# Kernel tuning notes

Measured on AMD Instinct MI355X. Metric: run time of the kernel, lower is better.

Reference implementation:

```python
import jax, jax.numpy as jnp
import numpy as np

BASE_RES = 0.2
RES_FACTOR = (1.0 - BASE_RES) * 0.9
N_ATOMS = 1024
LATENT = 128
WINDOW = 512
HOP = WINDOW // 2
RES_SAMPLES = 32768
N_FRAMES = RES_SAMPLES // HOP  # 128


def setup_inputs() -> dict:
    key = jax.random.key(0)
    ks = jax.random.split(key, 6)
    x = jax.random.normal(ks[0], (16, 64, LATENT), dtype=jnp.float32)
    W_sel = jax.random.normal(ks[1], (N_ATOMS, LATENT), dtype=jnp.float32) * 0.1
    b_sel = jnp.zeros((N_ATOMS,), dtype=jnp.float32)
    W_mom = jax.random.normal(ks[2], (N_FRAMES, LATENT), dtype=jnp.float32) * 0.1
    b_mom = jnp.zeros((N_FRAMES,), dtype=jnp.float32)
    atoms = jax.random.normal(ks[3], (N_ATOMS, RES_SAMPLES), dtype=jnp.float32) * 0.01
    return {"x": x, "W_sel": W_sel, "b_sel": b_sel, "W_mom": W_mom, "b_mom": b_mom, "atoms": atoms}


def _hann_periodic(n):
    # torch.hann_window default (periodic=True)
    return 0.5 * (1.0 - jnp.cos(2.0 * jnp.pi * jnp.arange(n) / n))


def reference(x, W_sel, b_sel, W_mom, b_mom, atoms):
    # momentum: sigmoid -> affine -> log-cumsum-exp decay per frame
    mom = BASE_RES + jax.nn.sigmoid(jnp.einsum('bel,fl->bef', x, W_mom) + b_mom) * RES_FACTOR
    mom = jnp.exp(jnp.cumsum(jnp.log(1e-12 + mom), axis=-1))  # (B,E,F)

    # softmax atom selection and mixing
    sel = jax.nn.softmax(jnp.einsum('bel,al->bea', x, W_sel) + b_sel, axis=-1)
    res = jnp.einsum('bea,as->bes', sel, atoms)  # (B,E,S)

    # windowed_audio: pad by hop, unfold, apply hann window
    padded = jnp.pad(res, ((0, 0), (0, 0), (0, HOP)))
    idx = jnp.arange(N_FRAMES)[:, None] * HOP + jnp.arange(WINDOW)[None, :]
    frames = padded[..., idx] * _hann_periodic(WINDOW)  # (B,E,F,W)

    # per-frame unit norm, then momentum scaling
    norm = jnp.linalg.norm(frames, axis=-1, keepdims=True)
    frames = frames / (norm + 1e-8)
    frames = frames * mom[..., None]

    # overlap-add with hop = WINDOW//2 (no extra window)
    B, E = frames.shape[0], frames.shape[1]
    first = frames[..., :HOP].reshape(B, E, -1)
    second = frames[..., HOP:].reshape(B, E, -1)
    out = jnp.pad(first, ((0, 0), (0, 0), (0, HOP))) + jnp.pad(second, ((0, 0), (0, 0), (HOP, 0)))
    return out[..., :RES_SAMPLES], mom
```

## Files before the change

### kernel.cpp

```cpp
#include <hip/hip_runtime.h>


typedef __attribute__((ext_vector_type(8))) short short8;
typedef __attribute__((ext_vector_type(4))) float f32x4;

typedef __attribute__((address_space(1))) void GV;
typedef __attribute__((address_space(3))) void LV;

__device__ __forceinline__ unsigned short f2bf(float f) {
    union { float f; unsigned u; } c; c.f = f;
    unsigned u = c.u;
    u = (u + 0x7FFFu + ((u >> 16) & 1u)) >> 16;
    return (unsigned short)u;
}
__device__ __forceinline__ float bf2f(unsigned short h) {
    union { unsigned u; float f; } c; c.u = ((unsigned)h) << 16; return c.f;
}

__global__ __launch_bounds__(256) void k_convert(
        const float* __restrict__ x, const float* __restrict__ Wsel,
        const float* __restrict__ Wmom,
        unsigned short* __restrict__ xbf, unsigned short* __restrict__ wbf,
        float* __restrict__ WmomT) {
    const int i = (blockIdx.x * 256 + threadIdx.x) * 4;
    {
        float4 v = *(const float4*)(x + i);
        uint2 q;
        q.x = (unsigned)f2bf(v.x) | ((unsigned)f2bf(v.y) << 16);
        q.y = (unsigned)f2bf(v.z) | ((unsigned)f2bf(v.w) << 16);
        *(uint2*)(xbf + i) = q;
    }
    {
        float4 v = *(const float4*)(Wsel + i);
        uint2 q;
        q.x = (unsigned)f2bf(v.x) | ((unsigned)f2bf(v.y) << 16);
        q.y = (unsigned)f2bf(v.z) | ((unsigned)f2bf(v.w) << 16);
        *(uint2*)(wbf + i) = q;
    }
    if (blockIdx.x < 8) {
        const int f  = blockIdx.x * 16 + (threadIdx.x >> 4);
        const int kc = (threadIdx.x & 15) * 8;
        float4 a = *(const float4*)(Wmom + (size_t)f * 128 + kc);
        float4 b = *(const float4*)(Wmom + (size_t)f * 128 + kc + 4);
        WmomT[(kc + 0) * 128 + f] = a.x; WmomT[(kc + 1) * 128 + f] = a.y;
        WmomT[(kc + 2) * 128 + f] = a.z; WmomT[(kc + 3) * 128 + f] = a.w;
        WmomT[(kc + 4) * 128 + f] = b.x; WmomT[(kc + 5) * 128 + f] = b.y;
        WmomT[(kc + 6) * 128 + f] = b.z; WmomT[(kc + 7) * 128 + f] = b.w;
    }
}

__global__ __launch_bounds__(256) void k_head_gemm(
        const unsigned short* __restrict__ A, const unsigned short* __restrict__ Bm,
        float* __restrict__ logits) {
    __shared__ __align__(16) unsigned short lA[128 * 32];
    __shared__ __align__(16) unsigned short lB[128 * 32];
    const int tid = threadIdx.x;
    const int wave = tid >> 6;
    const int lane = tid & 63;
    const int l15 = lane & 15, quad = lane >> 4;
    const int i0 = blockIdx.x * 128;
    const int j0 = blockIdx.y * 128;
    const int wi = wave >> 1, wj = wave & 1;
    const int rsel = lane >> 2;
    const int koff = (lane & 3) * 8;

    f32x4 acc[4][4] = {};

    for (int kt = 0; kt < 4; ++kt) {
        const int kbase = kt * 32;
#pragma unroll
        for (int c = 0; c < 2; ++c) {
            const int row = c * 64 + wave * 16 + rsel;
            const unsigned short* ga = A + (size_t)(i0 + row) * 128 + kbase + koff;
            const unsigned short* gb = Bm + (size_t)(j0 + row) * 128 + kbase + koff;
            unsigned short* la = lA + (c * 64 + wave * 16) * 32;
            unsigned short* lb = lB + (c * 64 + wave * 16) * 32;
            __builtin_amdgcn_global_load_lds((GV*)ga, (LV*)la, 16, 0, 0);
            __builtin_amdgcn_global_load_lds((GV*)gb, (LV*)lb, 16, 0, 0);
        }
        __syncthreads();

        short8 af[4], bf[4];
#pragma unroll
        for (int ti = 0; ti < 4; ++ti)
            af[ti] = *(const short8*)(lA + (wi * 64 + ti * 16 + l15) * 32 + quad * 8);
#pragma unroll
        for (int tj = 0; tj < 4; ++tj)
            bf[tj] = *(const short8*)(lB + (wj * 64 + tj * 16 + l15) * 32 + quad * 8);
#pragma unroll
        for (int ti = 0; ti < 4; ++ti)
#pragma unroll
            for (int tj = 0; tj < 4; ++tj)
                acc[ti][tj] = __builtin_amdgcn_mfma_f32_16x16x32_bf16(
                    af[ti], bf[tj], acc[ti][tj], 0, 0, 0);
        __syncthreads();
    }

#pragma unroll
    for (int ti = 0; ti < 4; ++ti) {
#pragma unroll
        for (int tj = 0; tj < 4; ++tj) {
            const int mrow = j0 + wj * 64 + tj * 16 + l15;
            const int abase = i0 + wi * 64 + ti * 16 + quad * 4;
            f32x4 v = acc[ti][tj];
            float4 o; o.x = v[0]; o.y = v[1]; o.z = v[2]; o.w = v[3];
            *(float4*)(logits + (size_t)mrow * 1024 + abase) = o;
        }
    }
}

__global__ __launch_bounds__(256) void k_softmax_mom(
        const float* __restrict__ logits_g, const float* __restrict__ bsel,
        const float* __restrict__ x, const float* __restrict__ WmomT,
        const float* __restrict__ bmom, unsigned short* __restrict__ sel,
        float* __restrict__ momout) {
    __shared__ float xs[128];
    __shared__ float logits[1024];
    __shared__ float mvals[128];
    __shared__ float wred[4];
    __shared__ float sstat[2];
    const int tid = threadIdx.x;
    const int m = blockIdx.x;

    if (tid < 32) *(float4*)&xs[tid * 4] = *(const float4*)(x + (size_t)m * 128 + tid * 4);
    for (int a = tid; a < 1024; a += 256)
        logits[a] = logits_g[(size_t)m * 1024 + a] + bsel[a];
    __syncthreads();

    if (tid < 128) {
        float acc = bmom[tid];
#pragma unroll 8
        for (int k = 0; k < 128; ++k)
            acc += xs[k] * WmomT[k * 128 + tid];
        float sig = 1.f / (1.f + __expf(-acc));
        mvals[tid] = 0.2f + sig * 0.72f;
    }

    float mx = -1e30f;
    for (int a = tid; a < 1024; a += 256) mx = fmaxf(mx, logits[a]);
#pragma unroll
    for (int off = 32; off; off >>= 1) mx = fmaxf(mx, __shfl_xor(mx, off, 64));
    if ((tid & 63) == 0) wred[tid >> 6] = mx;
    __syncthreads();
    if (tid == 0) sstat[0] = fmaxf(fmaxf(wred[0], wred[1]), fmaxf(wred[2], wred[3]));
    __syncthreads();
    mx = sstat[0];

    float psum = 0.f;
    for (int a = tid; a < 1024; a += 256) {
        float e = __expf(logits[a] - mx);
        logits[a] = e;
        psum += e;
    }
#pragma unroll
    for (int off = 32; off; off >>= 1) psum += __shfl_xor(psum, off, 64);
    if ((tid & 63) == 0) wred[tid >> 6] = psum;
    __syncthreads();
    if (tid == 0) sstat[1] = wred[0] + wred[1] + wred[2] + wred[3];
    __syncthreads();
    const float inv = 1.f / sstat[1];
    for (int a = tid; a < 1024; a += 256)
        sel[(size_t)m * 1024 + a] = f2bf(logits[a] * inv);

    if (tid == 0) {
        float p = 1.f;
        for (int f = 0; f < 128; ++f) {
            p *= (mvals[f] + 1e-12f);
            momout[(size_t)m * 128 + f] = p;
        }
    }
}

__global__ __launch_bounds__(256) void k_transpose(
        const float* __restrict__ atoms, unsigned short* __restrict__ atomsT) {
    __shared__ float t[64][65];
    const int tid = threadIdx.x;
    const int s0 = blockIdx.x * 64;
    const int a0 = blockIdx.y * 64;

    {
        const int r0 = tid >> 4;
        const int c4 = (tid & 15) * 4;
        for (int rr = r0; rr < 64; rr += 16) {
            float4 v = *(const float4*)(atoms + (size_t)(a0 + rr) * 32768 + s0 + c4);
            t[rr][c4] = v.x; t[rr][c4 + 1] = v.y; t[rr][c4 + 2] = v.z; t[rr][c4 + 3] = v.w;
        }
    }
    __syncthreads();
    {
        const int sl = tid >> 2;
        const int seg = (tid & 3) * 16;
        unsigned short* dst = atomsT + (size_t)(s0 + sl) * 1024 + a0 + seg;
        unsigned pk[8];
#pragma unroll
        for (int i = 0; i < 16; i += 2) {
            unsigned short h0 = f2bf(t[seg + i][sl]);
            unsigned short h1 = f2bf(t[seg + i + 1][sl]);
            pk[i >> 1] = (unsigned)h0 | ((unsigned)h1 << 16);
        }
        uint4 q0; q0.x = pk[0]; q0.y = pk[1]; q0.z = pk[2]; q0.w = pk[3];
        uint4 q1; q1.x = pk[4]; q1.y = pk[5]; q1.z = pk[6]; q1.w = pk[7];
        *(uint4*)(dst) = q0;
        *(uint4*)(dst + 8) = q1;
    }
}

__global__ __launch_bounds__(512, 2) void k_gemm(
        const unsigned short* __restrict__ A, const unsigned short* __restrict__ Bm,
        unsigned short* __restrict__ res) {
    __shared__ __align__(16) unsigned short smem[65536];
    const int tid = threadIdx.x;
    const int lane = tid & 63;
    const int wave = tid >> 6;
    const int l15 = lane & 15, quad = lane >> 4;
    const int wm = wave >> 2;
    const int wn = wave & 3;

    const int wg = ((blockIdx.x & 7) << 6) | (blockIdx.x >> 3);
    const int m_tile = wg & 3;
    const int s_tile = wg >> 2;
    const int i0 = s_tile << 8;
    const int j0 = m_tile << 8;

    const unsigned short* gA[2];
    const unsigned short* gB[2];
    int st_ld[2];
#pragma unroll
    for (int r = 0; r < 2; ++r) {
        const int qq = r * 64 + (tid >> 3);
        const int Gs = (tid & 7) ^ (qq & 7);
        const int row = 2 * qq + (Gs >> 2);
        const int g8 = (Gs & 3) * 8;
        st_ld[r] = r * 4096 + tid * 8;
        gA[r] = A  + (size_t)(i0 + row) * 1024 + g8;
        gB[r] = Bm + (size_t)(j0 + row) * 1024 + g8;
    }

    const int Gp = (((l15 & 1) << 2) | quad) ^ (l15 >> 1);
    const int aoff = wm * 4096 + (l15 >> 1) * 64 + Gp * 8;
    const int boff = wn * 2048 + (l15 >> 1) * 64 + Gp * 8;

#define STAGE(T) {                                                            \
    unsigned short* bb = smem + ((T) & 3) * 16384;                            \
    const int kb = (T) * 32;                                                  \
    __builtin_amdgcn_global_load_lds((GV*)(gA[0] + kb), (LV*)(bb + st_ld[0]), 16, 0, 0); \
    __builtin_amdgcn_global_load_lds((GV*)(gA[1] + kb), (LV*)(bb + st_ld[1]), 16, 0, 0); \
    __builtin_amdgcn_global_load_lds((GV*)(gB[0] + kb), (LV*)(bb + 8192 + st_ld[0]), 16, 0, 0); \
    __builtin_amdgcn_global_load_lds((GV*)(gB[1] + kb), (LV*)(bb + 8192 + st_ld[1]), 16, 0, 0); }

#define TILE(T, VMC, DOSTAGE) {                                               \
    asm volatile("s_waitcnt vmcnt(" VMC ")" ::: "memory");                    \
    __builtin_amdgcn_s_barrier();                                             \
    if (DOSTAGE) STAGE((T) + 3);                                              \
    const unsigned short* bufA = smem + ((T) & 3) * 16384;                    \
    const unsigned short* bufB = bufA + 8192;                                 \
    short8 a8[8], b8[4];                                                      \
    _Pragma("unroll")                                                         \
    for (int tj = 0; tj < 4; ++tj)                                            \
        b8[tj] = *(const short8*)(bufB + boff + tj * 512);                    \
    _Pragma("unroll")                                                         \
    for (int ti = 0; ti < 8; ++ti)                                            \
        a8[ti] = *(const short8*)(bufA + aoff + ti * 512);                    \
    __builtin_amdgcn_s_setprio(1);                                            \
    _Pragma("unroll")                                                         \
    for (int ti = 0; ti < 8; ++ti)                                            \
    _Pragma("unroll")                                                         \
    for (int tj = 0; tj < 4; ++tj)                                            \
        acc[ti][tj] = __builtin_amdgcn_mfma_f32_16x16x32_bf16(                \
            a8[ti], b8[tj], acc[ti][tj], 0, 0, 0);                            \
    __builtin_amdgcn_s_setprio(0); }

    f32x4 acc[8][4] = {};

    STAGE(0); STAGE(1); STAGE(2);
    for (int t = 0; t < 29; ++t)
        TILE(t, "8", true);
    TILE(29, "8", false);
    TILE(30, "4", false);
    TILE(31, "0", false);

#undef TILE
#undef STAGE

    asm volatile("s_waitcnt lgkmcnt(0)" ::: "memory");
    __builtin_amdgcn_s_barrier();
#pragma unroll
    for (int ti = 0; ti < 8; ++ti) {
#pragma unroll
        for (int tj = 0; tj < 4; ++tj) {
            const int mloc = wn * 64 + tj * 16 + l15;
            const int g = wm * 32 + ti * 4 + quad;
            const int gs = g ^ (mloc & 15);
            f32x4 v = acc[ti][tj];
            uint2 q2;
            q2.x = (unsigned)f2bf(v[0]) | ((unsigned)f2bf(v[1]) << 16);
            q2.y = (unsigned)f2bf(v[2]) | ((unsigned)f2bf(v[3]) << 16);
            *(uint2*)(smem + mloc * 256 + gs * 4) = q2;
        }
    }
    asm volatile("s_waitcnt lgkmcnt(0)" ::: "memory");
    __builtin_amdgcn_s_barrier();
    {
        const int r = tid >> 1;
        const int h = tid & 1;
        unsigned short* grow = res + (size_t)(j0 + r) * 32768 + i0 + h * 128;
        const unsigned short* lrow = smem + r * 256;
        const int rx = r & 15;
#pragma unroll
        for (int j = 0; j < 32; j += 2) {
            const int g0 = (h * 32 + j) ^ rx;
            const int g1 = (h * 32 + j + 1) ^ rx;
            uint2 u0 = *(const uint2*)(lrow + g0 * 4);
            uint2 u1 = *(const uint2*)(lrow + g1 * 4);
            uint4 q; q.x = u0.x; q.y = u0.y; q.z = u1.x; q.w = u1.y;
            *(uint4*)(grow + j * 4) = q;
        }
    }
}

__global__ __launch_bounds__(256) void k_final(
        const unsigned short* __restrict__ res, const float* __restrict__ mom,
        float* __restrict__ out) {
    __shared__ float hann[512];
    __shared__ float P0[128];
    __shared__ float P1[128];
    __shared__ float scl[129];
    const int tid = threadIdx.x;
    const int m = blockIdx.x;
    const unsigned short* row = res + (size_t)m * 32768;

    hann[tid]       = 0.5f * (1.f - cosf(6.283185307179586f * (float)tid / 512.f));
    hann[tid + 256] = 0.5f * (1.f - cosf(6.283185307179586f * (float)(tid + 256) / 512.f));
    if (tid == 0) scl[0] = 0.f;
    __syncthreads();

    const int wave = tid >> 6, lane = tid & 63;
    const int ih = (lane & 31) * 8;
    for (int cp = wave; cp < 64; cp += 4) {
        const unsigned short* p = row + cp * 512 + lane * 8;
        uint4 q = *(const uint4*)p;
        float s0 = 0.f, s1 = 0.f;
        const unsigned w[4] = {q.x, q.y, q.z, q.w};
#pragma unroll
        for (int j = 0; j < 4; ++j) {
            float v0 = bf2f((unsigned short)w[j]);
            float v1 = bf2f((unsigned short)(w[j] >> 16));
            float a0 = v0 * hann[ih + j * 2],       a1 = v1 * hann[ih + j * 2 + 1];
            float b0 = v0 * hann[256 + ih + j * 2], b1 = v1 * hann[256 + ih + j * 2 + 1];
            s0 += a0 * a0 + a1 * a1;
            s1 += b0 * b0 + b1 * b1;
        }
#pragma unroll
        for (int off = 1; off <= 16; off <<= 1) {
            s0 += __shfl_xor(s0, off, 64);
            s1 += __shfl_xor(s1, off, 64);
        }
        if ((lane & 31) == 0) {
            const int c = 2 * cp + (lane >> 5);
            P0[c] = s0; P1[c] = s1;
        }
    }
    __syncthreads();
    if (tid < 128) {
        const float n2 = P0[tid] + ((tid < 127) ? P1[tid + 1] : 0.f);
        scl[tid + 1] = mom[(size_t)m * 128 + tid] / (sqrtf(n2) + 1e-8f);
    }
    __syncthreads();

#pragma unroll 4
    for (int j = 0; j < 32; ++j) {
        const int s0 = j * 1024 + tid * 4;
        const int f1 = s0 >> 8, i1 = s0 & 255;
        const float sc1 = scl[f1 + 1];
        const float sc0 = scl[f1];
        uint2 rp = *(const uint2*)(row + s0);
        float4 o;
        o.x = bf2f((unsigned short)rp.x)         * (hann[i1]     * sc1 + hann[i1 + 256] * sc0);
        o.y = bf2f((unsigned short)(rp.x >> 16)) * (hann[i1 + 1] * sc1 + hann[i1 + 257] * sc0);
        o.z = bf2f((unsigned short)rp.y)         * (hann[i1 + 2] * sc1 + hann[i1 + 258] * sc0);
        o.w = bf2f((unsigned short)(rp.y >> 16)) * (hann[i1 + 3] * sc1 + hann[i1 + 259] * sc0);
        *(float4*)(out + (size_t)m * 32768 + s0) = o;
    }
}

extern "C" void kernel_launch(void* const* d_in, const int* in_sizes, int n_in,
                              void* d_out, int out_size, void* d_ws, size_t ws_size,
                              hipStream_t stream) {
    const float* x     = (const float*)d_in[0];
    const float* Wsel  = (const float*)d_in[1];
    const float* bsel  = (const float*)d_in[2];
    const float* Wmom  = (const float*)d_in[3];
    const float* bmom  = (const float*)d_in[4];
    const float* atoms = (const float*)d_in[5];

    float* out    = (float*)d_out;
    float* momout = out + (size_t)1024 * 32768;

    unsigned char* ws = (unsigned char*)d_ws;
    unsigned short* atomsT = (unsigned short*)(ws);
    unsigned short* sel    = (unsigned short*)(ws + 67108864);
    unsigned short* res    = (unsigned short*)(ws + 69206016);
    float*          logits = (float*)res;
    unsigned short* xbf    = (unsigned short*)(ws + 69206016 + 4194304);
    unsigned short* wbf    = (unsigned short*)(ws + 69206016 + 4194304 + 262144);
    float*          WmomT  = (float*)(ws + 69206016 + 4194304 + 524288);

    k_convert<<<128, 256, 0, stream>>>(x, Wsel, Wmom, xbf, wbf, WmomT);
    k_head_gemm<<<dim3(8, 8), 256, 0, stream>>>(wbf, xbf, logits);
    k_softmax_mom<<<1024, 256, 0, stream>>>(logits, bsel, x, WmomT, bmom, sel, momout);
    k_transpose<<<dim3(512, 16), 256, 0, stream>>>(atoms, atomsT);
    k_gemm<<<512, 512, 0, stream>>>(atomsT, sel, res);
    k_final<<<1024, 256, 0, stream>>>(res, momout, out);
}
```

Baseline: 387.7 us.

## Split GEMM tile into two half-phases interleaving LDS reads, staging, and MFMAs

Restructures the bf16 GEMM main loop so each K-tile runs in two halves. Each half loads half the A fragments, issues half of the next-stage global-to-LDS loads (A then B), and runs 16 MFMAs, with extra barriers between the halves. The wait on the vector-memory counter moves to the middle of the tile and the tail wait counts are adjusted. The aim is a ping-pong schedule that overlaps memory issue with MFMA work and lowers register pressure, at the cost of more barriers per tile.

```diff
diff --git a/kernel.cpp b/kernel.cpp
--- a/kernel.cpp
+++ b/kernel.cpp
@@ -240,47 +240,74 @@
     const int aoff = wm * 4096 + (l15 >> 1) * 64 + Gp * 8;
     const int boff = wn * 2048 + (l15 >> 1) * 64 + Gp * 8;
 
-#define STAGE(T) {                                                            \
+#define STAGE_A(T) {                                                          \
     unsigned short* bb = smem + ((T) & 3) * 16384;                            \
     const int kb = (T) * 32;                                                  \
     __builtin_amdgcn_global_load_lds((GV*)(gA[0] + kb), (LV*)(bb + st_ld[0]), 16, 0, 0); \
-    __builtin_amdgcn_global_load_lds((GV*)(gA[1] + kb), (LV*)(bb + st_ld[1]), 16, 0, 0); \
+    __builtin_amdgcn_global_load_lds((GV*)(gA[1] + kb), (LV*)(bb + st_ld[1]), 16, 0, 0); }
+
+#define STAGE_B(T) {                                                          \
+    unsigned short* bb = smem + ((T) & 3) * 16384;                            \
+    const int kb = (T) * 32;                                                  \
     __builtin_amdgcn_global_load_lds((GV*)(gB[0] + kb), (LV*)(bb + 8192 + st_ld[0]), 16, 0, 0); \
     __builtin_amdgcn_global_load_lds((GV*)(gB[1] + kb), (LV*)(bb + 8192 + st_ld[1]), 16, 0, 0); }
 
 #define TILE(T, VMC, DOSTAGE) {                                               \
-    asm volatile("s_waitcnt vmcnt(" VMC ")" ::: "memory");                    \
-    __builtin_amdgcn_s_barrier();                                             \
-    if (DOSTAGE) STAGE((T) + 3);                                              \
     const unsigned short* bufA = smem + ((T) & 3) * 16384;                    \
     const unsigned short* bufB = bufA + 8192;                                 \
-    short8 a8[8], b8[4];                                                      \
+    short8 a8[4], b8[4];                                                      \
+                     \
     _Pragma("unroll")                                                         \
     for (int tj = 0; tj < 4; ++tj)                                            \
         b8[tj] = *(const short8*)(bufB + boff + tj * 512);                    \
     _Pragma("unroll")                                                         \
-    for (int ti = 0; ti < 8; ++ti)                                            \
+    for (int ti = 0; ti < 4; ++ti)                                            \
         a8[ti] = *(const short8*)(bufA + aoff + ti * 512);                    \
+    if (DOSTAGE) STAGE_A((T) + 3);                                            \
+    __builtin_amdgcn_s_barrier();                                             \
     __builtin_amdgcn_s_setprio(1);                                            \
     _Pragma("unroll")                                                         \
-    for (int ti = 0; ti < 8; ++ti)                                            \
+    for (int ti = 0; ti < 4; ++ti)                                            \
     _Pragma("unroll")                                                         \
     for (int tj = 0; tj < 4; ++tj)                                            \
         acc[ti][tj] = __builtin_amdgcn_mfma_f32_16x16x32_bf16(                \
             a8[ti], b8[tj], acc[ti][tj], 0, 0, 0);                            \
-    __builtin_amdgcn_s_setprio(0); }
+    __builtin_amdgcn_s_setprio(0);                                            \
+    __builtin_amdgcn_s_barrier();                                             \
+             \
+    _Pragma("unroll")                                                         \
+    for (int ti = 0; ti < 4; ++ti)                                            \
+        a8[ti] = *(const short8*)(bufA + aoff + (ti + 4) * 512);              \
+    if (DOSTAGE) STAGE_B((T) + 3);                                            \
+    asm volatile("s_waitcnt vmcnt(" VMC ")" ::: "memory");                    \
+    __builtin_amdgcn_s_barrier();                                             \
+    __builtin_amdgcn_s_setprio(1);                                            \
+    _Pragma("unroll")                                                         \
+    for (int ti = 0; ti < 4; ++ti)                                            \
+    _Pragma("unroll")                                                         \
+    for (int tj = 0; tj < 4; ++tj)                                            \
+        acc[ti + 4][tj] = __builtin_amdgcn_mfma_f32_16x16x32_bf16(            \
+            a8[ti], b8[tj], acc[ti + 4][tj], 0, 0, 0);                        \
+    __builtin_amdgcn_s_setprio(0);                                            \
+    __builtin_amdgcn_s_barrier(); }
 
     f32x4 acc[8][4] = {};
 
-    STAGE(0); STAGE(1); STAGE(2);
+    STAGE_A(0); STAGE_B(0);
+    STAGE_A(1); STAGE_B(1);
+    STAGE_A(2); STAGE_B(2);
+    asm volatile("s_waitcnt vmcnt(8)" ::: "memory");
+    __builtin_amdgcn_s_barrier();
+
     for (int t = 0; t < 29; ++t)
         TILE(t, "8", true);
-    TILE(29, "8", false);
-    TILE(30, "4", false);
+    TILE(29, "4", false);
+    TILE(30, "0", false);
     TILE(31, "0", false);
 
 #undef TILE
-#undef STAGE
+#undef STAGE_A
+#undef STAGE_B
 
     asm volatile("s_waitcnt lgkmcnt(0)" ::: "memory");
     __builtin_amdgcn_s_barrier();
```

After: 390.7 us. About the same (+0.8%).

## Restructure main GEMM to 4 waves with 128x128 per-wave tiles and double buffering

Applied to the files above, without the earlier changes.

The big bf16 GEMM workgroup drops from 8 waves to 4. Each wave now computes an 8x8 grid of 16x16 MFMA tiles instead of 8x4, which raises register-level reuse of the A and B fragments. The LDS pipeline goes from 4-stage to 2-stage double buffering, with an extra barrier after the fragment loads so the next stage can overwrite the buffer. The epilogue writes the 256x256 output tile in two halves through half the LDS. The cost is much higher accumulator register pressure (256 floats per lane), fewer waves to hide latency, and shallower prefetch.

```diff
diff --git a/kernel.cpp b/kernel.cpp
--- a/kernel.cpp
+++ b/kernel.cpp
@@ -205,16 +205,16 @@
     }
 }
 
-__global__ __launch_bounds__(512, 2) void k_gemm(
+__global__ __launch_bounds__(256, 1) void k_gemm(
         const unsigned short* __restrict__ A, const unsigned short* __restrict__ Bm,
         unsigned short* __restrict__ res) {
-    __shared__ __align__(16) unsigned short smem[65536];
+    __shared__ __align__(16) unsigned short smem[32768];
     const int tid = threadIdx.x;
     const int lane = tid & 63;
     const int wave = tid >> 6;
     const int l15 = lane & 15, quad = lane >> 4;
-    const int wm = wave >> 2;
-    const int wn = wave & 3;
+    const int wm = wave >> 1;
+    const int wn = wave & 1;
 
     const int wg = ((blockIdx.x & 7) << 6) | (blockIdx.x >> 3);
     const int m_tile = wg & 3;
@@ -222,99 +222,108 @@
     const int i0 = s_tile << 8;
     const int j0 = m_tile << 8;
 
-    const unsigned short* gA[2];
-    const unsigned short* gB[2];
-    int st_ld[2];
-#pragma unroll
-    for (int r = 0; r < 2; ++r) {
-        const int qq = r * 64 + (tid >> 3);
+    const unsigned short* gA[4];
+    const unsigned short* gB[4];
+    int st_ld[4];
+#pragma unroll
+    for (int r = 0; r < 4; ++r) {
+        const int qq = r * 32 + (tid >> 3);
         const int Gs = (tid & 7) ^ (qq & 7);
         const int row = 2 * qq + (Gs >> 2);
         const int g8 = (Gs & 3) * 8;
-        st_ld[r] = r * 4096 + tid * 8;
+        st_ld[r] = r * 2048 + tid * 8;
         gA[r] = A  + (size_t)(i0 + row) * 1024 + g8;
         gB[r] = Bm + (size_t)(j0 + row) * 1024 + g8;
     }
 
     const int Gp = (((l15 & 1) << 2) | quad) ^ (l15 >> 1);
     const int aoff = wm * 4096 + (l15 >> 1) * 64 + Gp * 8;
-    const int boff = wn * 2048 + (l15 >> 1) * 64 + Gp * 8;
+    const int boff = wn * 4096 + (l15 >> 1) * 64 + Gp * 8;
 
 #define STAGE(T) {                                                            \
-    unsigned short* bb = smem + ((T) & 3) * 16384;                            \
+    unsigned short* bb = smem + ((T) & 1) * 16384;                            \
     const int kb = (T) * 32;                                                  \
-    __builtin_amdgcn_global_load_lds((GV*)(gA[0] + kb), (LV*)(bb + st_ld[0]), 16, 0, 0); \
-    __builtin_amdgcn_global_load_lds((GV*)(gA[1] + kb), (LV*)(bb + st_ld[1]), 16, 0, 0); \
-    __builtin_amdgcn_global_load_lds((GV*)(gB[0] + kb), (LV*)(bb + 8192 + st_ld[0]), 16, 0, 0); \
-    __builtin_amdgcn_global_load_lds((GV*)(gB[1] + kb), (LV*)(bb + 8192 + st_ld[1]), 16, 0, 0); }
+    _Pragma("unroll")                                                         \
+    for (int r = 0; r < 4; ++r) {                                             \
+        __builtin_amdgcn_global_load_lds((GV*)(gA[r] + kb),                   \
+            (LV*)(bb + st_ld[r]), 16, 0, 0);                                  \
+        __builtin_amdgcn_global_load_lds((GV*)(gB[r] + kb),                   \
+            (LV*)(bb + 8192 + st_ld[r]), 16, 0, 0);                           \
+    } }
 
 #define TILE(T, VMC, DOSTAGE) {                                               \
     asm volatile("s_waitcnt vmcnt(" VMC ")" ::: "memory");                    \
     __builtin_amdgcn_s_barrier();                                             \
-    if (DOSTAGE) STAGE((T) + 3);                                              \
-    const unsigned short* bufA = smem + ((T) & 3) * 16384;                    \
+    const unsigned short* bufA = smem + ((T) & 1) * 16384;                    \
     const unsigned short* bufB = bufA + 8192;                                 \
-    short8 a8[8], b8[4];                                                      \
+    short8 a8[8], b8[8];                                                      \
     _Pragma("unroll")                                                         \
-    for (int tj = 0; tj < 4; ++tj)                                            \
+    for (int tj = 0; tj < 8; ++tj)                                            \
         b8[tj] = *(const short8*)(bufB + boff + tj * 512);                    \
     _Pragma("unroll")                                                         \
     for (int ti = 0; ti < 8; ++ti)                                            \
         a8[ti] = *(const short8*)(bufA + aoff + ti * 512);                    \
+    asm volatile("s_waitcnt lgkmcnt(0)" ::: "memory");                        \
+    __builtin_amdgcn_s_barrier();                                             \
+    if (DOSTAGE) STAGE((T) + 2);                                              \
     __builtin_amdgcn_s_setprio(1);                                            \
     _Pragma("unroll")                                                         \
     for (int ti = 0; ti < 8; ++ti)                                            \
     _Pragma("unroll")                                                         \
-    for (int tj = 0; tj < 4; ++tj)                                            \
+    for (int tj = 0; tj < 8; ++tj)                                            \
         acc[ti][tj] = __builtin_amdgcn_mfma_f32_16x16x32_bf16(                \
             a8[ti], b8[tj], acc[ti][tj], 0, 0, 0);                            \
     __builtin_amdgcn_s_setprio(0); }
 
-    f32x4 acc[8][4] = {};
-
-    STAGE(0); STAGE(1); STAGE(2);
-    for (int t = 0; t < 29; ++t)
+    f32x4 acc[8][8] = {};
+
+    STAGE(0); STAGE(1);
+    for (int t = 0; t < 30; ++t)
         TILE(t, "8", true);
-    TILE(29, "8", false);
-    TILE(30, "4", false);
+    TILE(30, "8", false);
     TILE(31, "0", false);
 
 #undef TILE
 #undef STAGE
 
-    asm volatile("s_waitcnt lgkmcnt(0)" ::: "memory");
-    __builtin_amdgcn_s_barrier();
-#pragma unroll
-    for (int ti = 0; ti < 8; ++ti) {
-#pragma unroll
-        for (int tj = 0; tj < 4; ++tj) {
-            const int mloc = wn * 64 + tj * 16 + l15;
-            const int g = wm * 32 + ti * 4 + quad;
-            const int gs = g ^ (mloc & 15);
-            f32x4 v = acc[ti][tj];
-            uint2 q2;
-            q2.x = (unsigned)f2bf(v[0]) | ((unsigned)f2bf(v[1]) << 16);
-            q2.y = (unsigned)f2bf(v[2]) | ((unsigned)f2bf(v[3]) << 16);
-            *(uint2*)(smem + mloc * 256 + gs * 4) = q2;
-        }
-    }
-    asm volatile("s_waitcnt lgkmcnt(0)" ::: "memory");
-    __builtin_amdgcn_s_barrier();
-    {
-        const int r = tid >> 1;
-        const int h = tid & 1;
-        unsigned short* grow = res + (size_t)(j0 + r) * 32768 + i0 + h * 128;
-        const unsigned short* lrow = smem + r * 256;
-        const int rx = r & 15;
-#pragma unroll
-        for (int j = 0; j < 32; j += 2) {
-            const int g0 = (h * 32 + j) ^ rx;
-            const int g1 = (h * 32 + j + 1) ^ rx;
-            uint2 u0 = *(const uint2*)(lrow + g0 * 4);
-            uint2 u1 = *(const uint2*)(lrow + g1 * 4);
-            uint4 q; q.x = u0.x; q.y = u0.y; q.z = u1.x; q.w = u1.y;
-            *(uint4*)(grow + j * 4) = q;
-        }
+    for (int h = 0; h < 2; ++h) {
+        __builtin_amdgcn_s_barrier();
+        if (wn == h) {
+#pragma unroll
+            for (int ti = 0; ti < 8; ++ti) {
+#pragma unroll
+                for (int tj = 0; tj < 8; ++tj) {
+                    const int mloc = tj * 16 + l15;
+                    const int g = wm * 32 + ti * 4 + quad;
+                    const int gs = g ^ (mloc & 15);
+                    f32x4 v = acc[ti][tj];
+                    uint2 q2;
+                    q2.x = (unsigned)f2bf(v[0]) | ((unsigned)f2bf(v[1]) << 16);
+                    q2.y = (unsigned)f2bf(v[2]) | ((unsigned)f2bf(v[3]) << 16);
+                    *(uint2*)(smem + mloc * 256 + gs * 4) = q2;
+                }
+            }
+        }
+        asm volatile("s_waitcnt lgkmcnt(0)" ::: "memory");
+        __builtin_amdgcn_s_barrier();
+        {
+            const int r = tid >> 1;
+            const int h2 = tid & 1;
+            unsigned short* grow = res + (size_t)(j0 + h * 128 + r) * 32768
+                                       + i0 + h2 * 128;
+            const unsigned short* lrow = smem + r * 256;
+            const int rx = r & 15;
+#pragma unroll
+            for (int j = 0; j < 32; j += 2) {
+                const int g0 = (h2 * 32 + j) ^ rx;
+                const int g1 = (h2 * 32 + j + 1) ^ rx;
+                uint2 u0 = *(const uint2*)(lrow + g0 * 4);
+                uint2 u1 = *(const uint2*)(lrow + g1 * 4);
+                uint4 q; q.x = u0.x; q.y = u0.y; q.z = u1.x; q.w = u1.y;
+                *(uint4*)(grow + j * 4) = q;
+            }
+        }
+        asm volatile("s_waitcnt lgkmcnt(0)" ::: "memory");
     }
 }
 
@@ -409,6 +418,6 @@
     k_head_gemm<<<dim3(8, 8), 256, 0, stream>>>(wbf, xbf, logits);
     k_softmax_mom<<<1024, 256, 0, stream>>>(logits, bsel, x, WmomT, bmom, sel, momout);
     k_transpose<<<dim3(512, 16), 256, 0, stream>>>(atoms, atomsT);
-    k_gemm<<<512, 512, 0, stream>>>(atomsT, sel, res);
+    k_gemm<<<512, 256, 0, stream>>>(atomsT, sel, res);
     k_final<<<1024, 256, 0, stream>>>(res, momout, out);
 }
```

New measurement: 393.8 us. No clear change (+1.6%).
